# Performance work log

Hardware: AMD Instinct MI355X
Metric: run time of the kernel (lower is better)

## Reference

```python
import jax, jax.numpy as jnp
import numpy as np

N = 100000   # nodes
E = 1600000  # edges
F = 128      # input/hidden dim
C = 3        # classes
G = 64       # graphs in batch


def setup_inputs() -> dict:
    key = jax.random.key(0)
    ks = jax.random.split(key, 12)
    s = 1.0 / np.sqrt(F)
    return {
        "x": jax.random.normal(ks[0], (N, F), dtype=jnp.float32),
        "edge_index": jax.random.randint(ks[1], (2, E), 0, N, dtype=jnp.int64),
        "batch": jnp.sort(jax.random.randint(ks[2], (N,), 0, G, dtype=jnp.int64)),
        "W1": jax.random.normal(ks[3], (F, F), dtype=jnp.float32) * s,
        "b1": jnp.zeros((F,), dtype=jnp.float32),
        "W2": jax.random.normal(ks[4], (F, F), dtype=jnp.float32) * s,
        "b2": jnp.zeros((F,), dtype=jnp.float32),
        "W3": jax.random.normal(ks[5], (F, F), dtype=jnp.float32) * s,
        "b3": jnp.zeros((F,), dtype=jnp.float32),
        "Wc": jax.random.normal(ks[6], (F, C), dtype=jnp.float32) * s,
        "bc": jnp.zeros((C,), dtype=jnp.float32),
    }


def reference(x, edge_index, batch, W1, b1, W2, b2, W3, b3, Wc, bc):
    n = x.shape[0]
    src, dst = edge_index[0], edge_index[1]
    # GCN adds self-loops: A_hat = A + I
    loops = jnp.arange(n, dtype=src.dtype)
    src_a = jnp.concatenate([src, loops])
    dst_a = jnp.concatenate([dst, loops])
    # symmetric normalization D^-1/2 (A+I) D^-1/2 (in-degree incl. self-loop)
    deg = jax.ops.segment_sum(jnp.ones_like(dst_a, dtype=x.dtype), dst_a, num_segments=n)
    dis = jnp.where(deg > 0, jax.lax.rsqrt(deg), 0.0)
    norm = dis[src_a] * dis[dst_a]  # [E+N]

    def gcn_conv(h, W, b):
        h = h @ W                                    # [N, F']
        msg = h[src_a] * norm[:, None]               # gather + scale
        agg = jax.ops.segment_sum(msg, dst_a, num_segments=n)  # scatter-add
        return agg + b

    h = jax.nn.relu(gcn_conv(x, W1, b1))   # dropout = identity in eval mode
    h = jax.nn.relu(gcn_conv(h, W2, b2))
    h = jax.nn.relu(gcn_conv(h, W3, b3))

    # global_mean_pool over graph ids
    sums = jax.ops.segment_sum(h, batch, num_segments=G)
    cnt = jax.ops.segment_sum(jnp.ones((n,), dtype=h.dtype), batch, num_segments=G)
    pooled = sums / jnp.maximum(cnt, 1.0)[:, None]
    return pooled @ Wc + bc
```

## Files before the change

kernel.cpp:

```cpp
#include <hip/hip_runtime.h>
#include <cstdint>
#include <cstddef>

#define FDIM 128
#define CHUNK 4096
#define BSHIFT 8
#define BMASK 255
#define MAXB 512

typedef unsigned short ushort_t;
typedef __attribute__((ext_vector_type(8))) short short8;
typedef __attribute__((ext_vector_type(4))) float floatx4;

__device__ inline ushort_t f2bf(float f) {
  unsigned u = __float_as_uint(f);
  u += 0x7fffu + ((u >> 16) & 1u);
  return (ushort_t)(u >> 16);
}
__device__ inline float bf2f(ushort_t h) {
  return __uint_as_float((unsigned)h << 16);
}

__global__ __launch_bounds__(256) void k_histw(const int* __restrict__ dst, int e,
                                               int nb, int* __restrict__ chunkHist,
                                               int nch,
                                               const float* __restrict__ W1,
                                               const float* __restrict__ W2,
                                               const float* __restrict__ W3,
                                               ushort_t* __restrict__ wsw,
                                               int* __restrict__ counter) {
  if (blockIdx.x >= (unsigned)nch) {
    int b = blockIdx.x - nch;
    if (b == 0 && threadIdx.x == 0) *counter = 0;
    const float* W = (b == 0) ? W1 : (b == 1) ? W2 : W3;
    ushort_t* o = wsw + (size_t)b * 16384;
    for (int idx = threadIdx.x; idx < 16384; idx += 256) {
      int j = idx & 7;
      int lane = (idx >> 3) & 63;
      int ct = (idx >> 9) & 7;
      int kc = idx >> 12;
      int k = kc * 32 + (lane >> 4) * 8 + j;
      int col = (lane & 15) * 8 + ct;
      o[idx] = f2bf(W[k * FDIM + col]);
    }
    return;
  }
  __shared__ int h[MAXB];
  int c = blockIdx.x;
  int base = c * CHUNK;
  int end = min(base + CHUNK, e);
  for (int i = threadIdx.x; i < nb; i += 256) h[i] = 0;
  __syncthreads();
  for (int i = base + threadIdx.x; i < end; i += 256)
    atomicAdd(&h[dst[i] >> BSHIFT], 1);
  __syncthreads();
  for (int b = threadIdx.x; b < nb; b += 256)
    chunkHist[(size_t)c * nb + b] = h[b];
}

__global__ __launch_bounds__(512) void k_scan1(const int* __restrict__ chunkHist,
                                               int nchunks, int nb,
                                               int* __restrict__ chunkOff,
                                               int* __restrict__ bucketTotal,
                                               int* __restrict__ bucketBase,
                                               int* __restrict__ counter) {
  __shared__ int sb[512];
  int b = blockIdx.x;
  int t = threadIdx.x;
  int base = 0;
  for (int c0 = 0; c0 < nchunks; c0 += 512) {
    int c = c0 + t;
    int v = (c < nchunks) ? chunkHist[(size_t)c * nb + b] : 0;
    int x = v;
    sb[t] = x;
    __syncthreads();
    for (int off = 1; off < 512; off <<= 1) {
      int y = (t >= off) ? sb[t - off] : 0;
      __syncthreads();
      x += y;
      sb[t] = x;
      __syncthreads();
    }
    if (c < nchunks) chunkOff[(size_t)c * nb + b] = base + x - v;
    int tileTot = sb[511];
    __syncthreads();
    base += tileTot;
  }
  if (t == 0) {
    bucketTotal[b] = base;
    bucketBase[b] = atomicAdd(counter, base);
  }
}

__global__ __launch_bounds__(256) void k_bin(const int* __restrict__ src,
                                             const int* __restrict__ dst, int e, int nb,
                                             const int* __restrict__ chunkHist,
                                             const int* __restrict__ chunkOff,
                                             const int* __restrict__ bucketBase,
                                             unsigned* __restrict__ binned) {
  __shared__ unsigned sortedL[CHUNK];
  __shared__ int gtarget[CHUNK];
  __shared__ int lbase[MAXB], lcur[MAXB], gbase[MAXB];
  __shared__ int stmp[256];
  int c = blockIdx.x;
  int base = c * CHUNK;
  int end = min(base + CHUNK, e);
  for (int i = threadIdx.x; i < nb; i += 256) {
    lbase[i] = chunkHist[(size_t)c * nb + i];
    gbase[i] = bucketBase[i] + chunkOff[(size_t)c * nb + i];
  }
  __syncthreads();
  int carry = 0;
  for (int i0 = 0; i0 < nb; i0 += 256) {
    int i = i0 + threadIdx.x;
    int v = (i < nb) ? lbase[i] : 0;
    int x = v;
    stmp[threadIdx.x] = x;
    __syncthreads();
    for (int off = 1; off < 256; off <<= 1) {
      int y = (threadIdx.x >= off) ? stmp[threadIdx.x - off] : 0;
      __syncthreads();
      x += y;
      stmp[threadIdx.x] = x;
      __syncthreads();
    }
    if (i < nb) lbase[i] = carry + x - v;
    int tileTot = stmp[255];
    __syncthreads();
    carry += tileTot;
  }
  for (int i = threadIdx.x; i < nb; i += 256) lcur[i] = lbase[i];
  __syncthreads();
  for (int i = base + threadIdx.x; i < end; i += 256) {
    int d = dst[i];
    int sv = src[i];
    int b = d >> BSHIFT;
    int slot = atomicAdd(&lcur[b], 1);
    sortedL[slot] = ((unsigned)sv << BSHIFT) | (unsigned)(d & BMASK);
    gtarget[slot] = gbase[b] + (slot - lbase[b]);
  }
  __syncthreads();
  for (int i = threadIdx.x; i < end - base; i += 256)
    binned[gtarget[i]] = sortedL[i];
}

__global__ __launch_bounds__(256) void k_fill2(const unsigned* __restrict__ binned,
                                               const int* __restrict__ bucketBase,
                                               const int* __restrict__ bucketTotal,
                                               int n,
                                               int* __restrict__ rowStart,
                                               int* __restrict__ deg,
                                               float* __restrict__ dis,
                                               unsigned* __restrict__ colPacked) {
  __shared__ int h[256], sb[256], cur[256];
  int b = blockIdx.x;
  int s0 = bucketBase[b], s1 = s0 + bucketTotal[b];
  int nodeBase = b << BSHIFT;
  int t = threadIdx.x;
  h[t] = 0;
  __syncthreads();
  for (int i = s0 + t; i < s1; i += 256) atomicAdd(&h[binned[i] & BMASK], 1);
  __syncthreads();
  int v = h[t];
  int x = v;
  sb[t] = x;
  __syncthreads();
  for (int off = 1; off < 256; off <<= 1) {
    int y = (t >= off) ? sb[t - off] : 0;
    __syncthreads();
    x += y;
    sb[t] = x;
    __syncthreads();
  }
  int start = s0 + x - v;
  cur[t] = start;
  int node = nodeBase + t;
  if (node < n) {
    rowStart[node] = start;
    deg[node] = v;
    dis[node] = rsqrtf((float)(v + 1));
  }
  __syncthreads();
  for (int i = s0 + t; i < s1; i += 256) {
    unsigned en = binned[i];
    int slot = atomicAdd(&cur[en & BMASK], 1);
    colPacked[slot] = en >> BSHIFT;
  }
}

template <int INBF, int EDGW>
__global__ __launch_bounds__(256) void k_mm(const void* __restrict__ Ain,
                                            const ushort_t* __restrict__ Wsw,
                                            ushort_t* __restrict__ O, int n, int mmb,
                                            unsigned* __restrict__ colPacked, int e,
                                            const float* __restrict__ dis) {
  if (EDGW && blockIdx.x >= (unsigned)mmb) {
    int base = (blockIdx.x - mmb) * 2048 + threadIdx.x;
    for (int k = 0; k < 8; ++k) {
      int i = base + k * 256;
      if (i < e) {
        unsigned p = colPacked[i];
        colPacked[i] = p | ((unsigned)f2bf(dis[p]) << 17);
      }
    }
    return;
  }
  __shared__ ushort_t Bs[16384];
  int tid = threadIdx.x;
  for (int q = tid; q < 2048; q += 256)
    ((uint4*)Bs)[q] = ((const uint4*)Wsw)[q];
  __syncthreads();

  int w = tid >> 6;
  int lane = tid & 63;
  int quad = lane >> 4;
  int l15 = lane & 15;
  int rb = blockIdx.x * 128 + w * 32;
  const float* Af = (const float*)Ain;
  const ushort_t* Ab = (const ushort_t*)Ain;

  int row0 = rb + l15;
  int row1 = rb + 16 + l15;
  bool v0 = row0 < n, v1 = row1 < n;

  floatx4 acc[2][8];
#pragma unroll
  for (int rt = 0; rt < 2; ++rt)
#pragma unroll
    for (int ct = 0; ct < 8; ++ct) acc[rt][ct] = floatx4{0.f, 0.f, 0.f, 0.f};

#pragma unroll
  for (int kc = 0; kc < 4; ++kc) {
    int k0 = kc * 32 + quad * 8;
    short8 a0 = short8{0, 0, 0, 0, 0, 0, 0, 0};
    short8 a1 = short8{0, 0, 0, 0, 0, 0, 0, 0};
    if (INBF) {
      if (v0) a0 = *(const short8*)&Ab[(size_t)row0 * FDIM + k0];
      if (v1) a1 = *(const short8*)&Ab[(size_t)row1 * FDIM + k0];
    } else {
      if (v0) {
        float4 f0 = *(const float4*)&Af[(size_t)row0 * FDIM + k0];
        float4 f1 = *(const float4*)&Af[(size_t)row0 * FDIM + k0 + 4];
        a0 = short8{(short)f2bf(f0.x), (short)f2bf(f0.y), (short)f2bf(f0.z),
                    (short)f2bf(f0.w), (short)f2bf(f1.x), (short)f2bf(f1.y),
                    (short)f2bf(f1.z), (short)f2bf(f1.w)};
      }
      if (v1) {
        float4 f0 = *(const float4*)&Af[(size_t)row1 * FDIM + k0];
        float4 f1 = *(const float4*)&Af[(size_t)row1 * FDIM + k0 + 4];
        a1 = short8{(short)f2bf(f0.x), (short)f2bf(f0.y), (short)f2bf(f0.z),
                    (short)f2bf(f0.w), (short)f2bf(f1.x), (short)f2bf(f1.y),
                    (short)f2bf(f1.z), (short)f2bf(f1.w)};
      }
    }
#pragma unroll
    for (int ct = 0; ct < 8; ++ct) {
      short8 bf = *(const short8*)&Bs[((kc * 8 + ct) * 64 + lane) * 8];
      acc[0][ct] = __builtin_amdgcn_mfma_f32_16x16x32_bf16(a0, bf, acc[0][ct], 0, 0, 0);
      acc[1][ct] = __builtin_amdgcn_mfma_f32_16x16x32_bf16(a1, bf, acc[1][ct], 0, 0, 0);
    }
  }

#pragma unroll
  for (int rt = 0; rt < 2; ++rt) {
#pragma unroll
    for (int i = 0; i < 4; ++i) {
      int row = rb + rt * 16 + quad * 4 + i;
      if (row < n) {
        uint4 pk;
        pk.x = (unsigned)f2bf(acc[rt][0][i]) | ((unsigned)f2bf(acc[rt][1][i]) << 16);
        pk.y = (unsigned)f2bf(acc[rt][2][i]) | ((unsigned)f2bf(acc[rt][3][i]) << 16);
        pk.z = (unsigned)f2bf(acc[rt][4][i]) | ((unsigned)f2bf(acc[rt][5][i]) << 16);
        pk.w = (unsigned)f2bf(acc[rt][6][i]) | ((unsigned)f2bf(acc[rt][7][i]) << 16);
        *(uint4*)&O[(size_t)row * FDIM + l15 * 8] = pk;
      }
    }
  }
}

__global__ __launch_bounds__(256) void k_agg(const ushort_t* __restrict__ Hin,
                                             ushort_t* __restrict__ Hout,
                                             const int* __restrict__ rowStart,
                                             const int* __restrict__ degE,
                                             const unsigned* __restrict__ colPacked,
                                             const float* __restrict__ dis,
                                             const float* __restrict__ bias, int n) {
  int node = blockIdx.x * 8 + (threadIdx.x >> 5);
  int lane = threadIdx.x & 31;
  if (node >= n) return;
  const uint2* hin = (const uint2*)Hin;
  float di = dis[node];
  uint2 su = hin[(size_t)node * 32 + lane];
  float ws = di * di;
  float a0 = ws * __uint_as_float(su.x << 16);
  float a1 = ws * __uint_as_float(su.x & 0xffff0000u);
  float a2 = ws * __uint_as_float(su.y << 16);
  float a3 = ws * __uint_as_float(su.y & 0xffff0000u);
  int s0 = rowStart[node], cnt = degE[node];
#pragma unroll 4
  for (int j = 0; j < cnt; ++j) {
    unsigned pv = colPacked[s0 + j];
    int sidx = (int)(pv & 0x1ffffu);
    float w = di * __uint_as_float((pv >> 17) << 16);
    uint2 u = hin[(size_t)sidx * 32 + lane];
    a0 += w * __uint_as_float(u.x << 16);
    a1 += w * __uint_as_float(u.x & 0xffff0000u);
    a2 += w * __uint_as_float(u.y << 16);
    a3 += w * __uint_as_float(u.y & 0xffff0000u);
  }
  float4 b = ((const float4*)bias)[lane];
  a0 = fmaxf(a0 + b.x, 0.f);
  a1 = fmaxf(a1 + b.y, 0.f);
  a2 = fmaxf(a2 + b.z, 0.f);
  a3 = fmaxf(a3 + b.w, 0.f);
  uint2 o;
  o.x = (unsigned)f2bf(a0) | ((unsigned)f2bf(a1) << 16);
  o.y = (unsigned)f2bf(a2) | ((unsigned)f2bf(a3) << 16);
  ((uint2*)Hout)[(size_t)node * 32 + lane] = o;
}


__device__ inline int lower_bound_batch(const int* __restrict__ batch, int n, int g) {
  int lo = 0, hi = n;
  while (lo < hi) {
    int mid = (lo + hi) >> 1;
    if (batch[mid] < g) lo = mid + 1;
    else hi = mid;
  }
  return lo;
}

__global__ __launch_bounds__(128) void k_pool(const ushort_t* __restrict__ H,
                                              const int* __restrict__ batch, int n,
                                              float* __restrict__ partials,
                                              int g_count) {
  __shared__ int se[2];
  int g = blockIdx.x >> 4;
  int c = blockIdx.x & 15;
  if (threadIdx.x < 2)
    se[threadIdx.x] = lower_bound_batch(batch, n, g + (int)threadIdx.x);
  __syncthreads();
  int s = se[0], e = se[1];
  int chunk = (e - s + 15) >> 4;
  int ns = s + c * chunk;
  int ne = min(ns + chunk, e);
  float acc = 0.f;
  for (int i = ns; i < ne; ++i) acc += bf2f(H[(size_t)i * FDIM + threadIdx.x]);
  partials[((size_t)g * 16 + c) * FDIM + threadIdx.x] = acc;
}

__global__ __launch_bounds__(128) void k_final(const float* __restrict__ partials,
                                               const int* __restrict__ batch, int n,
                                               const float* __restrict__ Wc,
                                               const float* __restrict__ bc,
                                               float* __restrict__ out, int g_count) {
  __shared__ int se[2];
  __shared__ float red[6];
  int t = threadIdx.x;
  int g = blockIdx.x;
  if (t < 2) se[t] = lower_bound_batch(batch, n, g + t);
  __syncthreads();
  float inv = 1.0f / (float)max(se[1] - se[0], 1);
  float s = 0.f;
#pragma unroll
  for (int p = 0; p < 16; ++p) s += partials[((size_t)g * 16 + p) * FDIM + t];
  s *= inv;
#pragma unroll
  for (int c = 0; c < 3; ++c) {
    float v = s * Wc[t * 3 + c];
#pragma unroll
    for (int off = 1; off < 64; off <<= 1) v += __shfl_xor(v, off);
    if ((t & 63) == 0) red[(t >> 6) * 3 + c] = v;
  }
  __syncthreads();
  if (t < 3) out[g * 3 + t] = red[t] + red[3 + t] + bc[t];
}


extern "C" void kernel_launch(void* const* d_in, const int* in_sizes, int n_in,
                              void* d_out, int out_size, void* d_ws, size_t ws_size,
                              hipStream_t stream) {
  const float* x = (const float*)d_in[0];
  const int* edge = (const int*)d_in[1];
  const int* batch = (const int*)d_in[2];
  const float* W1 = (const float*)d_in[3];
  const float* b1 = (const float*)d_in[4];
  const float* W2 = (const float*)d_in[5];
  const float* b2 = (const float*)d_in[6];
  const float* W3 = (const float*)d_in[7];
  const float* b3 = (const float*)d_in[8];
  const float* Wc = (const float*)d_in[9];
  const float* bc = (const float*)d_in[10];
  float* out = (float*)d_out;

  const int N = in_sizes[0] / FDIM;
  const int E = in_sizes[1] / 2;
  const int G = out_size / 3;
  const int* src = edge;
  const int* dst = edge + E;

  const int NCH = (E + CHUNK - 1) / CHUNK;
  const int NB = (N + (1 << BSHIFT) - 1) >> BSHIFT;

  char* ws = (char*)d_ws;
  size_t off = 0;
  auto carve = [&](size_t bytes) -> void* {
    void* p = ws + off;
    off = (off + bytes + 255) & ~(size_t)255;
    return p;
  };
  ushort_t* h0 = (ushort_t*)carve((size_t)N * FDIM * 2);
  ushort_t* h1 = (ushort_t*)carve((size_t)N * FDIM * 2);
  unsigned* colPacked = (unsigned*)carve((size_t)E * 4);
  unsigned* binned = (unsigned*)carve((size_t)E * 4);
  int* chunkHist = (int*)carve((size_t)NCH * NB * 4);
  int* chunkOff = (int*)carve((size_t)NCH * NB * 4);
  int* bucketTotal = (int*)carve((size_t)NB * 4);
  int* bucketBase = (int*)carve((size_t)NB * 4);
  int* counter = (int*)carve(256);
  int* rowStart = (int*)carve((size_t)N * 4);
  int* deg = (int*)carve((size_t)N * 4);
  float* dis = (float*)carve((size_t)N * 4);
  float* partials = (float*)carve((size_t)G * 16 * FDIM * 4);
  ushort_t* wsw = (ushort_t*)carve((size_t)3 * 16384 * 2);
  (void)n_in;
  (void)ws_size;

  k_histw<<<NCH + 3, 256, 0, stream>>>(dst, E, NB, chunkHist, NCH, W1, W2, W3, wsw,
                                       counter);
  k_scan1<<<NB, 512, 0, stream>>>(chunkHist, NCH, NB, chunkOff, bucketTotal,
                                  bucketBase, counter);
  k_bin<<<NCH, 256, 0, stream>>>(src, dst, E, NB, chunkHist, chunkOff, bucketBase,
                                 binned);
  k_fill2<<<NB, 256, 0, stream>>>(binned, bucketBase, bucketTotal, N, rowStart, deg,
                                  dis, colPacked);

  int mmb = (N + 127) / 128;
  int ewb = (E + 2047) / 2048;
  int aggb = (N + 7) / 8;
  k_mm<0, 1><<<mmb + ewb, 256, 0, stream>>>(x, wsw, h0, N, mmb, colPacked, E, dis);
  k_agg<<<aggb, 256, 0, stream>>>(h0, h1, rowStart, deg, colPacked, dis, b1, N);
  k_mm<1, 0><<<mmb, 256, 0, stream>>>(h1, wsw + 16384, h0, N, mmb, nullptr, 0,
                                      nullptr);
  k_agg<<<aggb, 256, 0, stream>>>(h0, h1, rowStart, deg, colPacked, dis, b2, N);
  k_mm<1, 0><<<mmb, 256, 0, stream>>>(h1, wsw + 32768, h0, N, mmb, nullptr, 0,
                                      nullptr);
  k_agg<<<aggb, 256, 0, stream>>>(h0, h1, rowStart, deg, colPacked, dis, b3, N);

  k_pool<<<G * 16, 128, 0, stream>>>(h1, batch, N, partials, G);
  k_final<<<G, 128, 0, stream>>>(partials, batch, N, Wc, bc, out, G);
}
```

Before: 426.4 us.

## Fuse global mean pooling into the last aggregation kernel via atomics

The third aggregation kernel now accumulates its ReLU outputs straight into a per-graph pooled buffer. Blocks whose 8 nodes all belong to one graph first reduce in shared memory, and mixed blocks do global atomics. This removes the write and re-read of the final hidden matrix and the separate pooling kernel. In exchange it adds a memset, shared-memory atomics and about 12.5K global atomic bursts onto only 64 rows, which can contend and makes the float summation order nondeterministic.

New measurement: 451.6 us. +5.9%, slower.

```diff
diff --git a/kernel.cpp b/kernel.cpp
--- a/kernel.cpp
+++ b/kernel.cpp
@@ -278,45 +278,85 @@
   }
 }
 
+template <int POOL>
 __global__ __launch_bounds__(256) void k_agg(const ushort_t* __restrict__ Hin,
                                              ushort_t* __restrict__ Hout,
                                              const int* __restrict__ rowStart,
                                              const int* __restrict__ degE,
                                              const unsigned* __restrict__ colPacked,
                                              const float* __restrict__ dis,
-                                             const float* __restrict__ bias, int n) {
-  int node = blockIdx.x * 8 + (threadIdx.x >> 5);
-  int lane = threadIdx.x & 31;
-  if (node >= n) return;
-  const uint2* hin = (const uint2*)Hin;
-  float di = dis[node];
-  uint2 su = hin[(size_t)node * 32 + lane];
-  float ws = di * di;
-  float a0 = ws * __uint_as_float(su.x << 16);
-  float a1 = ws * __uint_as_float(su.x & 0xffff0000u);
-  float a2 = ws * __uint_as_float(su.y << 16);
-  float a3 = ws * __uint_as_float(su.y & 0xffff0000u);
-  int s0 = rowStart[node], cnt = degE[node];
+                                             const float* __restrict__ bias, int n,
+                                             const int* __restrict__ batch,
+                                             float* __restrict__ pooled) {
+  __shared__ float pbuf[FDIM];
+  __shared__ int guni;
+  int t = threadIdx.x;
+  int node = blockIdx.x * 8 + (t >> 5);
+  int lane = t & 31;
+  if (POOL) {
+    if (t < FDIM) pbuf[t] = 0.f;
+    if (t == 0) {
+      int nb0 = blockIdx.x * 8;
+      int nlast = min(nb0 + 7, n - 1);
+      int g0 = batch[nb0];
+      guni = (batch[nlast] == g0) ? g0 : -1;
+    }
+    __syncthreads();
+  }
+  bool active = node < n;
+  float a0 = 0.f, a1 = 0.f, a2 = 0.f, a3 = 0.f;
+  if (active) {
+    const uint2* hin = (const uint2*)Hin;
+    float di = dis[node];
+    uint2 su = hin[(size_t)node * 32 + lane];
+    float wsl = di * di;
+    a0 = wsl * __uint_as_float(su.x << 16);
+    a1 = wsl * __uint_as_float(su.x & 0xffff0000u);
+    a2 = wsl * __uint_as_float(su.y << 16);
+    a3 = wsl * __uint_as_float(su.y & 0xffff0000u);
+    int s0 = rowStart[node], cnt = degE[node];
 #pragma unroll 4
-  for (int j = 0; j < cnt; ++j) {
-    unsigned pv = colPacked[s0 + j];
-    int sidx = (int)(pv & 0x1ffffu);
-    float w = di * __uint_as_float((pv >> 17) << 16);
-    uint2 u = hin[(size_t)sidx * 32 + lane];
-    a0 += w * __uint_as_float(u.x << 16);
-    a1 += w * __uint_as_float(u.x & 0xffff0000u);
-    a2 += w * __uint_as_float(u.y << 16);
-    a3 += w * __uint_as_float(u.y & 0xffff0000u);
-  }
-  float4 b = ((const float4*)bias)[lane];
-  a0 = fmaxf(a0 + b.x, 0.f);
-  a1 = fmaxf(a1 + b.y, 0.f);
-  a2 = fmaxf(a2 + b.z, 0.f);
-  a3 = fmaxf(a3 + b.w, 0.f);
-  uint2 o;
-  o.x = (unsigned)f2bf(a0) | ((unsigned)f2bf(a1) << 16);
-  o.y = (unsigned)f2bf(a2) | ((unsigned)f2bf(a3) << 16);
-  ((uint2*)Hout)[(size_t)node * 32 + lane] = o;
+    for (int j = 0; j < cnt; ++j) {
+      unsigned pv = colPacked[s0 + j];
+      int sidx = (int)(pv & 0x1ffffu);
+      float wv = di * __uint_as_float((pv >> 17) << 16);
+      uint2 u = hin[(size_t)sidx * 32 + lane];
+      a0 += wv * __uint_as_float(u.x << 16);
+      a1 += wv * __uint_as_float(u.x & 0xffff0000u);
+      a2 += wv * __uint_as_float(u.y << 16);
+      a3 += wv * __uint_as_float(u.y & 0xffff0000u);
+    }
+    float4 b = ((const float4*)bias)[lane];
+    a0 = fmaxf(a0 + b.x, 0.f);
+    a1 = fmaxf(a1 + b.y, 0.f);
+    a2 = fmaxf(a2 + b.z, 0.f);
+    a3 = fmaxf(a3 + b.w, 0.f);
+  }
+  if (!POOL) {
+    if (active) {
+      uint2 o;
+      o.x = (unsigned)f2bf(a0) | ((unsigned)f2bf(a1) << 16);
+      o.y = (unsigned)f2bf(a2) | ((unsigned)f2bf(a3) << 16);
+      ((uint2*)Hout)[(size_t)node * 32 + lane] = o;
+    }
+    return;
+  }
+  if (active) {
+    if (guni >= 0) {
+      atomicAdd(&pbuf[lane * 4 + 0], a0);
+      atomicAdd(&pbuf[lane * 4 + 1], a1);
+      atomicAdd(&pbuf[lane * 4 + 2], a2);
+      atomicAdd(&pbuf[lane * 4 + 3], a3);
+    } else {
+      int g = batch[node];
+      atomicAdd(&pooled[(size_t)g * FDIM + lane * 4 + 0], a0);
+      atomicAdd(&pooled[(size_t)g * FDIM + lane * 4 + 1], a1);
+      atomicAdd(&pooled[(size_t)g * FDIM + lane * 4 + 2], a2);
+      atomicAdd(&pooled[(size_t)g * FDIM + lane * 4 + 3], a3);
+    }
+  }
+  __syncthreads();
+  if (guni >= 0 && t < FDIM) atomicAdd(&pooled[(size_t)guni * FDIM + t], pbuf[t]);
 }
 
 
@@ -330,26 +370,7 @@
   return lo;
 }
 
-__global__ __launch_bounds__(128) void k_pool(const ushort_t* __restrict__ H,
-                                              const int* __restrict__ batch, int n,
-                                              float* __restrict__ partials,
-                                              int g_count) {
-  __shared__ int se[2];
-  int g = blockIdx.x >> 4;
-  int c = blockIdx.x & 15;
-  if (threadIdx.x < 2)
-    se[threadIdx.x] = lower_bound_batch(batch, n, g + (int)threadIdx.x);
-  __syncthreads();
-  int s = se[0], e = se[1];
-  int chunk = (e - s + 15) >> 4;
-  int ns = s + c * chunk;
-  int ne = min(ns + chunk, e);
-  float acc = 0.f;
-  for (int i = ns; i < ne; ++i) acc += bf2f(H[(size_t)i * FDIM + threadIdx.x]);
-  partials[((size_t)g * 16 + c) * FDIM + threadIdx.x] = acc;
-}
-
-__global__ __launch_bounds__(128) void k_final(const float* __restrict__ partials,
+__global__ __launch_bounds__(128) void k_final(const float* __restrict__ pooled,
                                                const int* __restrict__ batch, int n,
                                                const float* __restrict__ Wc,
                                                const float* __restrict__ bc,
@@ -361,10 +382,7 @@
   if (t < 2) se[t] = lower_bound_batch(batch, n, g + t);
   __syncthreads();
   float inv = 1.0f / (float)max(se[1] - se[0], 1);
-  float s = 0.f;
-#pragma unroll
-  for (int p = 0; p < 16; ++p) s += partials[((size_t)g * 16 + p) * FDIM + t];
-  s *= inv;
+  float s = pooled[(size_t)g * FDIM + t] * inv;
 #pragma unroll
   for (int c = 0; c < 3; ++c) {
     float v = s * Wc[t * 3 + c];
@@ -421,10 +439,12 @@
   int* rowStart = (int*)carve((size_t)N * 4);
   int* deg = (int*)carve((size_t)N * 4);
   float* dis = (float*)carve((size_t)N * 4);
-  float* partials = (float*)carve((size_t)G * 16 * FDIM * 4);
+  float* pooled = (float*)carve((size_t)G * FDIM * 4);
   ushort_t* wsw = (ushort_t*)carve((size_t)3 * 16384 * 2);
   (void)n_in;
   (void)ws_size;
+
+  hipMemsetAsync(pooled, 0, (size_t)G * FDIM * 4, stream);
 
   k_histw<<<NCH + 3, 256, 0, stream>>>(dst, E, NB, chunkHist, NCH, W1, W2, W3, wsw,
                                        counter);
@@ -439,14 +459,16 @@
   int ewb = (E + 2047) / 2048;
   int aggb = (N + 7) / 8;
   k_mm<0, 1><<<mmb + ewb, 256, 0, stream>>>(x, wsw, h0, N, mmb, colPacked, E, dis);
-  k_agg<<<aggb, 256, 0, stream>>>(h0, h1, rowStart, deg, colPacked, dis, b1, N);
+  k_agg<0><<<aggb, 256, 0, stream>>>(h0, h1, rowStart, deg, colPacked, dis, b1, N,
+                                     batch, nullptr);
   k_mm<1, 0><<<mmb, 256, 0, stream>>>(h1, wsw + 16384, h0, N, mmb, nullptr, 0,
                                       nullptr);
-  k_agg<<<aggb, 256, 0, stream>>>(h0, h1, rowStart, deg, colPacked, dis, b2, N);
+  k_agg<0><<<aggb, 256, 0, stream>>>(h0, h1, rowStart, deg, colPacked, dis, b2, N,
+                                     batch, nullptr);
   k_mm<1, 0><<<mmb, 256, 0, stream>>>(h1, wsw + 32768, h0, N, mmb, nullptr, 0,
                                       nullptr);
-  k_agg<<<aggb, 256, 0, stream>>>(h0, h1, rowStart, deg, colPacked, dis, b3, N);
-
-  k_pool<<<G * 16, 128, 0, stream>>>(h1, batch, N, partials, G);
-  k_final<<<G, 128, 0, stream>>>(partials, batch, N, Wc, bc, out, G);
-}
+  k_agg<1><<<aggb, 256, 0, stream>>>(h0, h1, rowStart, deg, colPacked, dis, b3, N,
+                                     batch, pooled);
+
+  k_final<<<G, 128, 0, stream>>>(pooled, batch, N, Wc, bc, out, G);
+}
```
